# Kernel optimization log

Hardware: AMD Instinct MI355X
Metric: run time of the kernel (lower is better)

## Reference

```python
import jax, jax.numpy as jnp
import numpy as np

N_NODES = 100000
N_EDGES = 1600000
D_FEAT = 128
HIDDEN = 128
N_CLASSES = 10
NUM_GRAPHS = 64


def setup_inputs() -> dict:
    key = jax.random.key(0)
    ks = jax.random.split(key, 12)
    x = jax.random.normal(ks[0], (N_NODES, D_FEAT), dtype=jnp.float32)
    edge_index = jax.random.randint(ks[1], (2, N_EDGES), 0, N_NODES, dtype=jnp.int32)
    batch = jnp.sort(jax.random.randint(ks[2], (N_NODES,), 0, NUM_GRAPHS, dtype=jnp.int32))
    s = 1.0 / np.sqrt(HIDDEN)
    def lin(k, out_d, in_d):
        return jax.random.uniform(k, (out_d, in_d), jnp.float32, -s, s)
    return {
        "x": x,
        "edge_index": edge_index,
        "batch": batch,
        "W1l": lin(ks[3], HIDDEN, D_FEAT), "b1": jnp.zeros((HIDDEN,), jnp.float32),
        "W1r": lin(ks[4], HIDDEN, D_FEAT),
        "W2l": lin(ks[5], HIDDEN, HIDDEN), "b2": jnp.zeros((HIDDEN,), jnp.float32),
        "W2r": lin(ks[6], HIDDEN, HIDDEN),
        "W3l": lin(ks[7], HIDDEN, HIDDEN), "b3": jnp.zeros((HIDDEN,), jnp.float32),
        "W3r": lin(ks[8], HIDDEN, HIDDEN),
        "Wout": lin(ks[9], N_CLASSES, HIDDEN), "bout": jnp.zeros((N_CLASSES,), jnp.float32),
    }


def reference(x, edge_index, batch, W1l, b1, W1r, W2l, b2, W2r, W3l, b3, W3r, Wout, bout):
    src, dst = edge_index[0], edge_index[1]
    n = x.shape[0]

    def sage(h, Wl, b, Wr):
        # sum-aggregate neighbor features: scatter-add x[src] into dst rows
        agg = jax.ops.segment_sum(h[src], dst, num_segments=n)  # [N, d]
        return agg @ Wl.T + b + h @ Wr.T

    h = jax.nn.relu(sage(x, W1l, b1, W1r))
    h = jax.nn.relu(sage(h, W2l, b2, W2r))
    h = sage(h, W3l, b3, W3r)
    pooled = jax.ops.segment_sum(h, batch, num_segments=NUM_GRAPHS)  # [G, hidden]
    # dropout is identity in eval mode
    return pooled @ Wout.T + bout
```

## Files before the change

kernel.cpp:

```cpp
#include <hip/hip_runtime.h>
#include <hip/hip_bf16.h>

#define N_NODES  100000
#define N_EDGES  1600000
#define D_FEAT   128
#define HIDDEN   128
#define N_CLASSES 10
#define NUM_GRAPHS 64

#define NBUCK 250
#define NPB   400
#define BCAP  7168
#define GT    64
#define NPAD  100096
#define NTILES (NPAD / GT)

typedef __bf16 bf16x8 __attribute__((ext_vector_type(8)));
typedef float  f32x4  __attribute__((ext_vector_type(4)));

static __device__ __forceinline__ unsigned short f2bf(float f) {
    __bf16 b = (__bf16)f;
    return __builtin_bit_cast(unsigned short, b);
}

static __device__ __forceinline__ void async_copy16(void* lds, const void* g) {
    __builtin_amdgcn_global_load_lds(
        (const __attribute__((address_space(1))) void*)g,
        (__attribute__((address_space(3))) void*)lds, 16, 0, 0);
}

__global__ void conv_w6_kernel(const float* __restrict__ W0, const float* __restrict__ W1,
                               const float* __restrict__ W2, const float* __restrict__ W3,
                               const float* __restrict__ W4, const float* __restrict__ W5,
                               __bf16* __restrict__ out) {
    const float* Ws[6] = {W0, W1, W2, W3, W4, W5};
    int m = blockIdx.x >> 6;
    int i = (blockIdx.x & 63) * 256 + threadIdx.x;
    out[m * (HIDDEN * D_FEAT) + i] = (__bf16)Ws[m][i];
}

__global__ __launch_bounds__(256) void xconv_kernel(const float* __restrict__ x,
                                                    __bf16* __restrict__ out) {
    int i = blockIdx.x * 256 + threadIdx.x;
    bf16x8 o;
    if (i < N_NODES * 128 / 8) {
        float4 v0 = ((const float4*)x)[i * 2];
        float4 v1 = ((const float4*)x)[i * 2 + 1];
        o[0] = (__bf16)v0.x; o[1] = (__bf16)v0.y; o[2] = (__bf16)v0.z; o[3] = (__bf16)v0.w;
        o[4] = (__bf16)v1.x; o[5] = (__bf16)v1.y; o[6] = (__bf16)v1.z; o[7] = (__bf16)v1.w;
    } else {
        #pragma unroll
        for (int k = 0; k < 8; k++) o[k] = (__bf16)0.f;
    }
    if (i < NPAD * 128 / 8) ((bf16x8*)out)[i] = o;
}

__global__ __launch_bounds__(256) void bucket_scatter_kernel(const int* __restrict__ ei,
                                                             int* __restrict__ gcur,
                                                             int2* __restrict__ bkt) {
    __shared__ int h[NBUCK];
    __shared__ int lb[NBUCK];
    int t = threadIdx.x;
    const int CH = N_EDGES / 256;
    for (int i = t; i < NBUCK; i += 256) h[i] = 0;
    __syncthreads();
    int e0 = blockIdx.x * CH;
    for (int e = e0 + t; e < e0 + CH; e += 256) {
        int d = ei[N_EDGES + e];
        atomicAdd(&h[d / NPB], 1);
    }
    __syncthreads();
    for (int i = t; i < NBUCK; i += 256) {
        lb[i] = atomicAdd(&gcur[i], h[i]);
        h[i] = 0;
    }
    __syncthreads();
    for (int e = e0 + t; e < e0 + CH; e += 256) {
        int s = ei[e];
        int d = ei[N_EDGES + e];
        int bb = d / NPB;
        int pos = lb[bb] + atomicAdd(&h[bb], 1);
        if (pos < BCAP) bkt[(size_t)bb * BCAP + pos] = make_int2(s, d);
    }
}

__global__ __launch_bounds__(256) void bucket_csr_kernel(const int2* __restrict__ bkt,
                                                         const int* __restrict__ gcur,
                                                         int2* __restrict__ rpse,
                                                         int* __restrict__ csr_src) {
    const int b = blockIdx.x;
    const int n0 = b * NPB;
    const int base = b * BCAP;
    int m = gcur[b]; if (m > BCAP) m = BCAP;
    __shared__ int cnt[NPB];
    __shared__ int part[128];
    __shared__ int excl[NPB];
    int t = threadIdx.x;
    for (int i = t; i < NPB; i += 256) cnt[i] = 0;
    __syncthreads();
    for (int e = t; e < m; e += 256) {
        int2 p = bkt[base + e];
        atomicAdd(&cnt[p.y - n0], 1);
    }
    __syncthreads();
    int gs = 0;
    if (t < 100) { gs = cnt[4 * t] + cnt[4 * t + 1] + cnt[4 * t + 2] + cnt[4 * t + 3]; part[t] = gs; }
    else if (t < 128) part[t] = 0;
    __syncthreads();
    for (int off = 1; off < 128; off <<= 1) {
        int x = 0;
        if (t < 128 && t >= off) x = part[t - off];
        __syncthreads();
        if (t < 128) part[t] += x;
        __syncthreads();
    }
    if (t < 100) part[t] -= gs;
    __syncthreads();
    for (int i = t; i < NPB; i += 256) {
        int g = i >> 2;
        int e0 = part[g];
        for (int j = g * 4; j < i; j++) e0 += cnt[j];
        excl[i] = e0;
    }
    __syncthreads();
    for (int i = t; i < NPB; i += 256) {
        rpse[n0 + i] = make_int2(base + excl[i], base + excl[i] + cnt[i]);
    }
    __syncthreads();
    for (int i = t; i < NPB; i += 256) cnt[i] = excl[i];
    __syncthreads();
    for (int e = t; e < m; e += 256) {
        int2 p = bkt[base + e];
        int pos = base + atomicAdd(&cnt[p.y - n0], 1);
        csr_src[pos] = p.x;
    }
}

__global__ __launch_bounds__(256) void gather_kernel(
    const __bf16* __restrict__ h, const int2* __restrict__ rpse,
    const int* __restrict__ csr_src, __bf16* __restrict__ agg, int N)
{
    int nid = blockIdx.x * 16 + (threadIdx.x >> 4);
    if (nid >= N) return;
    int f8 = threadIdx.x & 15;
    int2 se = rpse[nid];

    float a[8] = {0.f, 0.f, 0.f, 0.f, 0.f, 0.f, 0.f, 0.f};

    int j = se.x;
    for (; j + 3 < se.y; j += 4) {
        int s0 = csr_src[j];
        int s1 = csr_src[j + 1];
        int s2 = csr_src[j + 2];
        int s3 = csr_src[j + 3];
        bf16x8 u0 = ((const bf16x8*)h)[(size_t)s0 * 16 + f8];
        bf16x8 u1 = ((const bf16x8*)h)[(size_t)s1 * 16 + f8];
        bf16x8 u2 = ((const bf16x8*)h)[(size_t)s2 * 16 + f8];
        bf16x8 u3 = ((const bf16x8*)h)[(size_t)s3 * 16 + f8];
        #pragma unroll
        for (int i = 0; i < 8; i++)
            a[i] += ((float)u0[i] + (float)u1[i]) + ((float)u2[i] + (float)u3[i]);
    }
    for (; j < se.y; j++) {
        int s0 = csr_src[j];
        bf16x8 u0 = ((const bf16x8*)h)[(size_t)s0 * 16 + f8];
        #pragma unroll
        for (int i = 0; i < 8; i++) a[i] += (float)u0[i];
    }
    bf16x8 o;
    #pragma unroll
    for (int i = 0; i < 8; i++) o[i] = (__bf16)a[i];
    ((bf16x8*)agg)[(size_t)nid * 16 + f8] = o;
}

template<bool RELU>
__global__ __launch_bounds__(256) void fused_gemm_kernel(
    const __bf16* __restrict__ hA,
    const __bf16* __restrict__ hG,
    const __bf16* __restrict__ Wl, const __bf16* __restrict__ Wr,
    const float* __restrict__ bias,
    __bf16* __restrict__ outp, int M)
{
    __shared__ __bf16 lds[2][GT * 128];

    const int tid  = threadIdx.x;
    const int wave = tid >> 6;
    const int lane = tid & 63;
    const int kq = lane >> 4;
    const int ln = lane & 15;
    const int node_base = blockIdx.x * GT;
    const int f_base = wave * 32;

    {
        const __bf16* gsrc = hG + (size_t)node_base * 128;
        const __bf16* asrc = hA + (size_t)node_base * 128;
        #pragma unroll
        for (int i = 0; i < 4; i++) {
            int u = i * 256 + tid;
            int row = u >> 4;
            int sc = (u & 15) ^ (row & 15);
            async_copy16(&lds[0][u * 8], gsrc + row * 128 + sc * 8);
            async_copy16(&lds[1][u * 8], asrc + row * 128 + sc * 8);
        }
    }

    bf16x8 wfragL[2][4], wfragR[2][4];
    #pragma unroll
    for (int t = 0; t < 2; t++) {
        int wrow = f_base + t * 16 + ln;
        #pragma unroll
        for (int kc = 0; kc < 4; kc++) {
            int k0 = kc * 32 + kq * 8;
            wfragL[t][kc] = *(const bf16x8*)(Wl + wrow * 128 + k0);
            wfragR[t][kc] = *(const bf16x8*)(Wr + wrow * 128 + k0);
        }
    }
    float4 bias4[2];
    bias4[0] = *(const float4*)(bias + f_base + kq * 4);
    bias4[1] = *(const float4*)(bias + f_base + 16 + kq * 4);

    __syncthreads();

    #pragma unroll 2
    for (int tau = 0; tau < GT / 16; tau++) {
        int r = tau * 16 + ln;
        bf16x8 gfrag[4], afrag[4];
        #pragma unroll
        for (int kc = 0; kc < 4; kc++) {
            int c = (4 * kc + kq) ^ ln;
            gfrag[kc] = *(const bf16x8*)&lds[0][r * 128 + c * 8];
            afrag[kc] = *(const bf16x8*)&lds[1][r * 128 + c * 8];
        }

        f32x4 acc[2] = {(f32x4)(0.f), (f32x4)(0.f)};
        #pragma unroll
        for (int kc = 0; kc < 4; kc++) {
            #pragma unroll
            for (int t = 0; t < 2; t++) {
                acc[t] = __builtin_amdgcn_mfma_f32_16x16x32_bf16(wfragL[t][kc], gfrag[kc], acc[t], 0, 0, 0);
                acc[t] = __builtin_amdgcn_mfma_f32_16x16x32_bf16(wfragR[t][kc], afrag[kc], acc[t], 0, 0, 0);
            }
        }

        int node = node_base + tau * 16 + ln;
        if (node < M) {
            size_t rowoff = (size_t)node * 128;
            #pragma unroll
            for (int t = 0; t < 2; t++) {
                int fc = f_base + t * 16 + kq * 4;
                ushort4 o;
                float v0 = acc[t][0] + bias4[t].x;
                float v1 = acc[t][1] + bias4[t].y;
                float v2 = acc[t][2] + bias4[t].z;
                float v3 = acc[t][3] + bias4[t].w;
                if (RELU) {
                    v0 = fmaxf(v0, 0.f); v1 = fmaxf(v1, 0.f);
                    v2 = fmaxf(v2, 0.f); v3 = fmaxf(v3, 0.f);
                }
                o.x = f2bf(v0); o.y = f2bf(v1); o.z = f2bf(v2); o.w = f2bf(v3);
                *(ushort4*)(outp + rowoff + fc) = o;
            }
        }
    }
}

__global__ __launch_bounds__(256) void pool_kernel(
    const __bf16* __restrict__ h, const int* __restrict__ batch,
    float* __restrict__ pooled, int N)
{
    int idx = blockIdx.x * 256 + threadIdx.x;
    int f = idx & 127;
    int chunk = idx >> 7;
    int n0 = chunk * 32;
    if (n0 >= N) return;
    int n1 = n0 + 32; if (n1 > N) n1 = N;
    int curb = batch[n0];
    float acc = 0.f;
    for (int n = n0; n < n1; n++) {
        int b = batch[n];
        if (b != curb) {
            unsafeAtomicAdd(&pooled[(size_t)curb * 128 + f], acc);
            acc = 0.f; curb = b;
        }
        acc += (float)h[(size_t)n * 128 + f];
    }
    unsafeAtomicAdd(&pooled[(size_t)curb * 128 + f], acc);
}

__global__ void final_gemm_kernel(
    const float* __restrict__ pooled, const float* __restrict__ Wout,
    const float* __restrict__ bout, float* __restrict__ out)
{
    int idx = blockIdx.x * 64 + threadIdx.x;
    if (idx < NUM_GRAPHS * N_CLASSES) {
        int g = idx / N_CLASSES;
        int c = idx % N_CLASSES;
        float acc = bout[c];
        for (int k = 0; k < HIDDEN; k++)
            acc += pooled[g * HIDDEN + k] * Wout[c * HIDDEN + k];
        out[idx] = acc;
    }
}

extern "C" void kernel_launch(void* const* d_in, const int* in_sizes, int n_in,
                              void* d_out, int out_size, void* d_ws, size_t ws_size,
                              hipStream_t stream) {
    const float* x     = (const float*)d_in[0];
    const int*   ei    = (const int*)d_in[1];
    const int*   batch = (const int*)d_in[2];
    const float* W1l = (const float*)d_in[3];
    const float* b1  = (const float*)d_in[4];
    const float* W1r = (const float*)d_in[5];
    const float* W2l = (const float*)d_in[6];
    const float* b2  = (const float*)d_in[7];
    const float* W2r = (const float*)d_in[8];
    const float* W3l = (const float*)d_in[9];
    const float* b3  = (const float*)d_in[10];
    const float* W3r = (const float*)d_in[11];
    const float* Wout = (const float*)d_in[12];
    const float* bout = (const float*)d_in[13];
    float* out = (float*)d_out;

    char* ws = (char*)d_ws;
    size_t off = 0;
    const size_t NB = (size_t)NPAD * 128 * sizeof(__bf16);
    __bf16* B0    = (__bf16*)(ws + off); off += NB;
    __bf16* B1    = (__bf16*)(ws + off); off += NB;
    __bf16* B2    = (__bf16*)(ws + off); off += NB;
    float* pooled = (float*)(ws + off);  off += (size_t)NUM_GRAPHS * HIDDEN * sizeof(float);
    __bf16* wbf   = (__bf16*)(ws + off); off += 6 * (size_t)HIDDEN * D_FEAT * sizeof(__bf16);
    int2* rpse    = (int2*)(ws + off);   off += (size_t)N_NODES * sizeof(int2);
    int* csr_src  = (int*)(ws + off);    off += (size_t)NBUCK * BCAP * sizeof(int);
    int2* bkt     = (int2*)(ws + off);   off += (size_t)NBUCK * BCAP * sizeof(int2);
    int* gcur     = (int*)(ws + off);    off += (NBUCK + 8) * sizeof(int);

    const int WSZ = HIDDEN * D_FEAT;

    conv_w6_kernel<<<6 * 64, 256, 0, stream>>>(W1l, W1r, W2l, W2r, W3l, W3r, wbf);
    xconv_kernel<<<NPAD * 128 / (256 * 8), 256, 0, stream>>>(x, B0);

    hipMemsetAsync(gcur, 0, NBUCK * sizeof(int), stream);
    bucket_scatter_kernel<<<256, 256, 0, stream>>>(ei, gcur, bkt);
    bucket_csr_kernel<<<NBUCK, 256, 0, stream>>>(bkt, gcur, rpse, csr_src);

    const int gath_grid = (N_NODES + 15) / 16;

    gather_kernel<<<gath_grid, 256, 0, stream>>>(B0, rpse, csr_src, B1, N_NODES);
    fused_gemm_kernel<true><<<NTILES, 256, 0, stream>>>(B0, B1, wbf + 0 * WSZ, wbf + 1 * WSZ, b1, B2, N_NODES);

    gather_kernel<<<gath_grid, 256, 0, stream>>>(B2, rpse, csr_src, B1, N_NODES);
    fused_gemm_kernel<true><<<NTILES, 256, 0, stream>>>(B2, B1, wbf + 2 * WSZ, wbf + 3 * WSZ, b2, B0, N_NODES);

    gather_kernel<<<gath_grid, 256, 0, stream>>>(B0, rpse, csr_src, B1, N_NODES);
    fused_gemm_kernel<false><<<NTILES, 256, 0, stream>>>(B0, B1, wbf + 4 * WSZ, wbf + 5 * WSZ, b3, B2, N_NODES);

    hipMemsetAsync(pooled, 0, (size_t)NUM_GRAPHS * HIDDEN * sizeof(float), stream);
    const int pool_grid = ((N_NODES + 31) / 32 * 128 + 255) / 256;
    pool_kernel<<<pool_grid, 256, 0, stream>>>(B2, batch, pooled, N_NODES);
    final_gemm_kernel<<<10, 64, 0, stream>>>(pooled, Wout, bout, out);
}
```

Before: 439.7 us.

## Fuse neighbor gather into per-layer GEMM and pack bucket entries into one int

Each SAGE layer now computes the neighbor sum for its 64-node tile straight into LDS inside the GEMM kernel, removing the separate gather kernel and the round trip of the aggregate buffer through global memory. Bucket entries are packed as src plus local dst in one 32-bit int, halving bucket traffic. The trade-off is that the fused kernel runs the gather with only 1563 blocks and its latency is no longer overlapped by a separate high-occupancy launch, so the GEMM waits on the gather inside each block. The GEMM tile loop is also fully unrolled.

```diff
diff --git a/kernel.cpp b/kernel.cpp
--- a/kernel.cpp
+++ b/kernel.cpp
@@ -57,7 +57,7 @@
 
 __global__ __launch_bounds__(256) void bucket_scatter_kernel(const int* __restrict__ ei,
                                                              int* __restrict__ gcur,
-                                                             int2* __restrict__ bkt) {
+                                                             int* __restrict__ bkt) {
     __shared__ int h[NBUCK];
     __shared__ int lb[NBUCK];
     int t = threadIdx.x;
@@ -80,11 +80,11 @@
         int d = ei[N_EDGES + e];
         int bb = d / NPB;
         int pos = lb[bb] + atomicAdd(&h[bb], 1);
-        if (pos < BCAP) bkt[(size_t)bb * BCAP + pos] = make_int2(s, d);
-    }
-}
-
-__global__ __launch_bounds__(256) void bucket_csr_kernel(const int2* __restrict__ bkt,
+        if (pos < BCAP) bkt[(size_t)bb * BCAP + pos] = s | ((d - bb * NPB) << 17);
+    }
+}
+
+__global__ __launch_bounds__(256) void bucket_csr_kernel(const int* __restrict__ bkt,
                                                          const int* __restrict__ gcur,
                                                          int2* __restrict__ rpse,
                                                          int* __restrict__ csr_src) {
@@ -99,8 +99,8 @@
     for (int i = t; i < NPB; i += 256) cnt[i] = 0;
     __syncthreads();
     for (int e = t; e < m; e += 256) {
-        int2 p = bkt[base + e];
-        atomicAdd(&cnt[p.y - n0], 1);
+        int p = bkt[base + e];
+        atomicAdd(&cnt[p >> 17], 1);
     }
     __syncthreads();
     int gs = 0;
@@ -130,53 +130,16 @@
     for (int i = t; i < NPB; i += 256) cnt[i] = excl[i];
     __syncthreads();
     for (int e = t; e < m; e += 256) {
-        int2 p = bkt[base + e];
-        int pos = base + atomicAdd(&cnt[p.y - n0], 1);
-        csr_src[pos] = p.x;
-    }
-}
-
-__global__ __launch_bounds__(256) void gather_kernel(
-    const __bf16* __restrict__ h, const int2* __restrict__ rpse,
-    const int* __restrict__ csr_src, __bf16* __restrict__ agg, int N)
-{
-    int nid = blockIdx.x * 16 + (threadIdx.x >> 4);
-    if (nid >= N) return;
-    int f8 = threadIdx.x & 15;
-    int2 se = rpse[nid];
-
-    float a[8] = {0.f, 0.f, 0.f, 0.f, 0.f, 0.f, 0.f, 0.f};
-
-    int j = se.x;
-    for (; j + 3 < se.y; j += 4) {
-        int s0 = csr_src[j];
-        int s1 = csr_src[j + 1];
-        int s2 = csr_src[j + 2];
-        int s3 = csr_src[j + 3];
-        bf16x8 u0 = ((const bf16x8*)h)[(size_t)s0 * 16 + f8];
-        bf16x8 u1 = ((const bf16x8*)h)[(size_t)s1 * 16 + f8];
-        bf16x8 u2 = ((const bf16x8*)h)[(size_t)s2 * 16 + f8];
-        bf16x8 u3 = ((const bf16x8*)h)[(size_t)s3 * 16 + f8];
-        #pragma unroll
-        for (int i = 0; i < 8; i++)
-            a[i] += ((float)u0[i] + (float)u1[i]) + ((float)u2[i] + (float)u3[i]);
-    }
-    for (; j < se.y; j++) {
-        int s0 = csr_src[j];
-        bf16x8 u0 = ((const bf16x8*)h)[(size_t)s0 * 16 + f8];
-        #pragma unroll
-        for (int i = 0; i < 8; i++) a[i] += (float)u0[i];
-    }
-    bf16x8 o;
-    #pragma unroll
-    for (int i = 0; i < 8; i++) o[i] = (__bf16)a[i];
-    ((bf16x8*)agg)[(size_t)nid * 16 + f8] = o;
+        int p = bkt[base + e];
+        int pos = base + atomicAdd(&cnt[p >> 17], 1);
+        csr_src[pos] = p & 131071;
+    }
 }
 
 template<bool RELU>
-__global__ __launch_bounds__(256) void fused_gemm_kernel(
-    const __bf16* __restrict__ hA,
-    const __bf16* __restrict__ hG,
+__global__ __launch_bounds__(256) void fused_layer_kernel(
+    const __bf16* __restrict__ h,
+    const int2* __restrict__ rpse, const int* __restrict__ csr_src,
     const __bf16* __restrict__ Wl, const __bf16* __restrict__ Wr,
     const float* __restrict__ bias,
     __bf16* __restrict__ outp, int M)
@@ -192,15 +155,13 @@
     const int f_base = wave * 32;
 
     {
-        const __bf16* gsrc = hG + (size_t)node_base * 128;
-        const __bf16* asrc = hA + (size_t)node_base * 128;
+        const __bf16* ssrc = h + (size_t)node_base * 128;
         #pragma unroll
         for (int i = 0; i < 4; i++) {
             int u = i * 256 + tid;
             int row = u >> 4;
             int sc = (u & 15) ^ (row & 15);
-            async_copy16(&lds[0][u * 8], gsrc + row * 128 + sc * 8);
-            async_copy16(&lds[1][u * 8], asrc + row * 128 + sc * 8);
+            async_copy16(&lds[1][u * 8], ssrc + row * 128 + sc * 8);
         }
     }
 
@@ -219,9 +180,47 @@
     bias4[0] = *(const float4*)(bias + f_base + kq * 4);
     bias4[1] = *(const float4*)(bias + f_base + 16 + kq * 4);
 
-    __syncthreads();
-
-    #pragma unroll 2
+    {
+        int f8 = tid & 15;
+        int ng = tid >> 4;
+        #pragma unroll 1
+        for (int rr = 0; rr < 4; rr++) {
+            int r = rr * 16 + ng;
+            int node = node_base + r;
+            float a[8] = {0.f, 0.f, 0.f, 0.f, 0.f, 0.f, 0.f, 0.f};
+            if (node < M) {
+                int2 se = rpse[node];
+                int j = se.x;
+                for (; j + 3 < se.y; j += 4) {
+                    int s0 = csr_src[j];
+                    int s1 = csr_src[j + 1];
+                    int s2 = csr_src[j + 2];
+                    int s3 = csr_src[j + 3];
+                    bf16x8 u0 = ((const bf16x8*)h)[(size_t)s0 * 16 + f8];
+                    bf16x8 u1 = ((const bf16x8*)h)[(size_t)s1 * 16 + f8];
+                    bf16x8 u2 = ((const bf16x8*)h)[(size_t)s2 * 16 + f8];
+                    bf16x8 u3 = ((const bf16x8*)h)[(size_t)s3 * 16 + f8];
+                    #pragma unroll
+                    for (int i = 0; i < 8; i++)
+                        a[i] += ((float)u0[i] + (float)u1[i]) + ((float)u2[i] + (float)u3[i]);
+                }
+                for (; j < se.y; j++) {
+                    int s0 = csr_src[j];
+                    bf16x8 u0 = ((const bf16x8*)h)[(size_t)s0 * 16 + f8];
+                    #pragma unroll
+                    for (int i = 0; i < 8; i++) a[i] += (float)u0[i];
+                }
+            }
+            bf16x8 o;
+            #pragma unroll
+            for (int i = 0; i < 8; i++) o[i] = (__bf16)a[i];
+            *(bf16x8*)&lds[0][r * 128 + (f8 ^ ng) * 8] = o;
+        }
+    }
+
+    __syncthreads();
+
+    #pragma unroll
     for (int tau = 0; tau < GT / 16; tau++) {
         int r = tau * 16 + ln;
         bf16x8 gfrag[4], afrag[4];
@@ -248,7 +247,6 @@
             #pragma unroll
             for (int t = 0; t < 2; t++) {
                 int fc = f_base + t * 16 + kq * 4;
-                ushort4 o;
                 float v0 = acc[t][0] + bias4[t].x;
                 float v1 = acc[t][1] + bias4[t].y;
                 float v2 = acc[t][2] + bias4[t].z;
@@ -257,6 +255,7 @@
                     v0 = fmaxf(v0, 0.f); v1 = fmaxf(v1, 0.f);
                     v2 = fmaxf(v2, 0.f); v3 = fmaxf(v3, 0.f);
                 }
+                ushort4 o;
                 o.x = f2bf(v0); o.y = f2bf(v1); o.z = f2bf(v2); o.w = f2bf(v3);
                 *(ushort4*)(outp + rowoff + fc) = o;
             }
@@ -325,13 +324,12 @@
     size_t off = 0;
     const size_t NB = (size_t)NPAD * 128 * sizeof(__bf16);
     __bf16* B0    = (__bf16*)(ws + off); off += NB;
-    __bf16* B1    = (__bf16*)(ws + off); off += NB;
     __bf16* B2    = (__bf16*)(ws + off); off += NB;
     float* pooled = (float*)(ws + off);  off += (size_t)NUM_GRAPHS * HIDDEN * sizeof(float);
     __bf16* wbf   = (__bf16*)(ws + off); off += 6 * (size_t)HIDDEN * D_FEAT * sizeof(__bf16);
     int2* rpse    = (int2*)(ws + off);   off += (size_t)N_NODES * sizeof(int2);
     int* csr_src  = (int*)(ws + off);    off += (size_t)NBUCK * BCAP * sizeof(int);
-    int2* bkt     = (int2*)(ws + off);   off += (size_t)NBUCK * BCAP * sizeof(int2);
+    int* bkt      = (int*)(ws + off);    off += (size_t)NBUCK * BCAP * sizeof(int);
     int* gcur     = (int*)(ws + off);    off += (NBUCK + 8) * sizeof(int);
 
     const int WSZ = HIDDEN * D_FEAT;
@@ -343,16 +341,9 @@
     bucket_scatter_kernel<<<256, 256, 0, stream>>>(ei, gcur, bkt);
     bucket_csr_kernel<<<NBUCK, 256, 0, stream>>>(bkt, gcur, rpse, csr_src);
 
-    const int gath_grid = (N_NODES + 15) / 16;
-
-    gather_kernel<<<gath_grid, 256, 0, stream>>>(B0, rpse, csr_src, B1, N_NODES);
-    fused_gemm_kernel<true><<<NTILES, 256, 0, stream>>>(B0, B1, wbf + 0 * WSZ, wbf + 1 * WSZ, b1, B2, N_NODES);
-
-    gather_kernel<<<gath_grid, 256, 0, stream>>>(B2, rpse, csr_src, B1, N_NODES);
-    fused_gemm_kernel<true><<<NTILES, 256, 0, stream>>>(B2, B1, wbf + 2 * WSZ, wbf + 3 * WSZ, b2, B0, N_NODES);
-
-    gather_kernel<<<gath_grid, 256, 0, stream>>>(B0, rpse, csr_src, B1, N_NODES);
-    fused_gemm_kernel<false><<<NTILES, 256, 0, stream>>>(B0, B1, wbf + 4 * WSZ, wbf + 5 * WSZ, b3, B2, N_NODES);
+    fused_layer_kernel<true><<<NTILES, 256, 0, stream>>>(B0, rpse, csr_src, wbf + 0 * WSZ, wbf + 1 * WSZ, b1, B2, N_NODES);
+    fused_layer_kernel<true><<<NTILES, 256, 0, stream>>>(B2, rpse, csr_src, wbf + 2 * WSZ, wbf + 3 * WSZ, b2, B0, N_NODES);
+    fused_layer_kernel<false><<<NTILES, 256, 0, stream>>>(B0, rpse, csr_src, wbf + 4 * WSZ, wbf + 5 * WSZ, b3, B2, N_NODES);
 
     hipMemsetAsync(pooled, 0, (size_t)NUM_GRAPHS * HIDDEN * sizeof(float), stream);
     const int pool_grid = ((N_NODES + 31) / 32 * 128 + 255) / 256;
```

Result: slower. 505.8 us (+15.0%).
